# Performance work log

Hardware: AMD Instinct MI355X
Metric: run time of the kernel (lower is better)

Reference implementation:

```python
import jax, jax.numpy as jnp
import numpy as np

B, N0, N1, FD, L, H = 4, 256, 256, 128, 3, 1
NG = N0 + N1            # nodes per graph
N = B * NG              # total nodes
EPS_BN = 1e-5
EPS_SM = 1e-16


def _build_edges():
    def perm_edges(n, off):
        idx = np.arange(n)
        a = np.repeat(idx, n); b = np.tile(idx, n)
        m = a != b
        return np.stack([a[m], b[m]]) + off
    e_intra = np.concatenate([perm_edges(N0, 0), perm_edges(N1, N0)], axis=1)
    a = np.arange(N0); b = np.arange(N0, N0 + N1)
    cross1 = np.stack([np.repeat(a, N1), np.tile(b, N0)])
    cross2 = np.stack([np.repeat(b, N0), np.tile(a, N1)])
    eg = np.concatenate([e_intra, cross1, cross2], axis=1)
    tg = np.concatenate([np.zeros(e_intra.shape[1], np.int32),
                         np.ones(cross1.shape[1] + cross2.shape[1], np.int32)])
    ei = np.concatenate([eg + g * NG for g in range(B)], axis=1).astype(np.int32)
    et = np.tile(tg, B).astype(np.int32)
    return jnp.asarray(ei), jnp.asarray(et)


def setup_inputs() -> dict:
    key = jax.random.key(0)
    ks = jax.random.split(key, 8)
    edge_index, edge_type = _build_edges()
    return {
        'desc0': jax.random.normal(ks[0], (B, FD, N0), jnp.float32),
        'desc1': jax.random.normal(ks[1], (B, FD, N1), jnp.float32),
        'W': jax.random.normal(ks[2], (L, 2, FD, H * FD), jnp.float32) * (1.0 / np.sqrt(FD)),
        'q': jax.random.normal(ks[3], (L, H * FD, H), jnp.float32) * 0.1,
        'k': jax.random.normal(ks[4], (L, H * FD, H), jnp.float32) * 0.1,
        'conv_b': jnp.zeros((L, FD), jnp.float32),
        'lin_W': jax.random.normal(ks[5], (L, FD, 2 * FD), jnp.float32) * (1.0 / np.sqrt(2 * FD)),
        'lin_b': jnp.zeros((L, FD), jnp.float32),
        'gamma': jnp.ones((L, FD), jnp.float32),
        'beta': jnp.zeros((L, FD), jnp.float32),
        'edge_index': edge_index,
        'edge_type': edge_type,
    }


def _forward(desc0, desc1, W, q, k, conv_b, lin_W, lin_b, gamma, beta, edge_index, edge_type):
    # x: [B, NG, FD] -> flattened batch graph [N, FD]
    x = jnp.concatenate([desc0, desc1], axis=2)        # [B, FD, NG]
    x = jnp.transpose(x, (0, 2, 1)).reshape(N, FD)
    src, dst = edge_index[0], edge_index[1]
    nlayers = W.shape[0]
    heads = q.shape[2]
    for l in range(nlayers):
        # relation-specific node projections (equiv to per-edge bmm with weight[edge_type])
        proj = jnp.einsum('nf,rfo->nro', x, W[l])       # [N, 2, H*FD]
        out_i = proj[dst, edge_type]                    # [E, H*FD]
        out_j = proj[src, edge_type]                    # [E, H*FD]
        alpha = jax.nn.leaky_relu(out_i @ q[l] + out_j @ k[l], 0.2)  # [E, H]
        # softmax over incoming edges of each destination node (across-relation)
        amax = jax.ops.segment_max(alpha, dst, num_segments=N)
        ex = jnp.exp(alpha - amax[dst])
        denom = jax.ops.segment_sum(ex, dst, num_segments=N)
        att = ex / (denom[dst] + EPS_SM)                # [E, H]
        msg = (att[:, :, None] * out_j.reshape(-1, heads, FD)).reshape(-1, heads * FD)
        agg = jax.ops.segment_sum(msg, dst, num_segments=N).reshape(N, heads, FD)
        m1 = jax.nn.relu(agg.mean(axis=1) + conv_b[l])  # concat=False -> mean over heads
        m2 = jnp.concatenate([x, m1], axis=1) @ lin_W[l].T + lin_b[l]
        mu = m2.mean(axis=0)
        var = ((m2 - mu) ** 2).mean(axis=0)             # biased var (BatchNorm training)
        m3 = (m2 - mu) / jnp.sqrt(var + EPS_BN) * gamma[l] + beta[l]
        x = x + m3
    x = x.reshape(B, NG, FD).transpose(0, 2, 1)         # [B, FD, NG]
    return x


def reference(desc0, desc1, W, q, k, conv_b, lin_W, lin_b, gamma, beta, edge_index, edge_type):
    x = _forward(desc0, desc1, W, q, k, conv_b, lin_W, lin_b, gamma, beta, edge_index, edge_type)
    return x[:, :, :N0], x[:, :, N0:]
```

## Files before the change

kernel.cpp:

```cpp
#include <hip/hip_runtime.h>

#define FD  128
#define NN  2048

#define OFF_X     0
#define OFF_PROJ  262144
#define OFF_QS    786432
#define OFF_KS    790528
#define OFF_SUMS  794624
#define OFF_LWT   800768
#define OFF_M2    899072

__device__ __forceinline__ int swizzle_n0(int bid) {
    int g    = (bid & 7) >> 1;
    int slot = ((bid >> 3) << 1) | (bid & 1);
    return g*512 + slot*8;
}

__device__ __forceinline__ void proj_qsks8(
    const float* __restrict__ W, const float* __restrict__ qv,
    const float* __restrict__ kv, float* __restrict__ ws,
    int l, int n0, int t, const float (*xs)[FD],
    float (*redp)[256], float* red)
{
    int kh = t >> 8, tp = t & 255;
    int rsel = tp >> 7, o = tp & 127;
    const float* Wl = W + ((size_t)(l*2 + rsel)*FD)*FD + o;
    float acc[8];
#pragma unroll
    for (int r = 0; r < 8; r++) acc[r] = 0.f;
    int kbase = kh * 64;
#pragma unroll
    for (int kk = 0; kk < 64; kk += 4) {
        int k4 = kbase + kk;
        float w0 = Wl[(k4+0)*FD], w1 = Wl[(k4+1)*FD];
        float w2 = Wl[(k4+2)*FD], w3 = Wl[(k4+3)*FD];
#pragma unroll
        for (int r = 0; r < 8; r++) {
            float4 xq = *(const float4*)&xs[r][k4];
            acc[r] += xq.x*w0 + xq.y*w1 + xq.z*w2 + xq.w*w3;
        }
    }
    if (kh == 1) {
#pragma unroll
        for (int r = 0; r < 8; r++) redp[r][tp] = acc[r];
    }
    __syncthreads();
    if (t < 256) {
#pragma unroll
        for (int r = 0; r < 8; r++) acc[r] += redp[r][tp];
#pragma unroll
        for (int r = 0; r < 8; r++)
            ws[OFF_PROJ + (size_t)(n0 + r)*256 + tp] = acc[r];

        float qq = qv[l*FD + o], kq = kv[l*FD + o];
        int lane = t & 63, w = t >> 6;
#pragma unroll
        for (int r = 0; r < 8; r++) {
            float vq = acc[r]*qq, vk = acc[r]*kq;
            for (int off = 32; off; off >>= 1) {
                vq += __shfl_xor(vq, off, 64);
                vk += __shfl_xor(vk, off, 64);
            }
            if (lane == 0) { red[w*16 + r*2] = vq; red[w*16 + r*2 + 1] = vk; }
        }
    }
    __syncthreads();
    if (t < 32) {
        int r = t & 7, rs = (t >> 3) & 1, wh = t >> 4;
        float v = red[(rs*2)*16 + r*2 + wh] + red[(rs*2 + 1)*16 + r*2 + wh];
        if (wh == 0) ws[OFF_QS + rs*NN + n0 + r] = v;
        else         ws[OFF_KS + rs*NN + n0 + r] = v;
    }
}

__global__ __launch_bounds__(512, 2) void k_pre(
    const float* __restrict__ d0, const float* __restrict__ d1,
    const float* __restrict__ W,  const float* __restrict__ qv,
    const float* __restrict__ kv, const float* __restrict__ linW,
    float* __restrict__ ws)
{
    int bid = blockIdx.x, t = threadIdx.x;
    if (bid >= 256) {
        if (bid < 280) {
            int vb = bid - 256;
#pragma unroll
            for (int i = 0; i < 8; i++) {
                int e = vb*4096 + i*512 + t;
                int l = e >> 15, rem = e & 32767;
                int o = rem >> 8, c = rem & 255;
                ws[OFF_LWT + l*32768 + c*FD + o] = linW[e];
            }
        } else {
            for (int i = t; i < 6144; i += 512) ws[OFF_SUMS + i] = 0.f;
        }
        return;
    }
    __shared__ __attribute__((aligned(16))) float xs[8][FD];
    __shared__ float redp[8][256];
    __shared__ float red[64];
    int n0 = swizzle_n0(bid);
#pragma unroll
    for (int i = 0; i < 2; i++) {
        int idx = t + i*512;
        int row = idx >> 7, f = idx & 127;
        int n = n0 + row, gg = n >> 9, ii = n & 511;
        float v = (ii < 256) ? d0[gg*32768 + f*256 + ii]
                             : d1[gg*32768 + f*256 + (ii - 256)];
        xs[row][f] = v;
        ws[OFF_X + (size_t)n*FD + f] = v;
    }
    __syncthreads();
    proj_qsks8(W, qv, kv, ws, 0, n0, t, xs, redp, red);
}

__global__ __launch_bounds__(512, 2) void k_bp(
    const float* __restrict__ W,     const float* __restrict__ qv,
    const float* __restrict__ kv,    const float* __restrict__ gamma,
    const float* __restrict__ beta,  float* __restrict__ ws, int l)
{
    __shared__ float scale[FD], shift[FD];
    __shared__ __attribute__((aligned(16))) float xs[8][FD];
    __shared__ float redp[8][256];
    __shared__ float red[64];
    int bid = blockIdx.x, t = threadIdx.x;
    int lp = l - 1;
    if (t < 128) {
        float s0 = 0.f, s1 = 0.f;
#pragma unroll
        for (int sl = 0; sl < 8; sl++) {
            s0 += ws[OFF_SUMS + lp*2048 + sl*256 + t];
            s1 += ws[OFF_SUMS + lp*2048 + sl*256 + 128 + t];
        }
        float mu  = s0 * (1.f/2048.f);
        float var = s1 * (1.f/2048.f) - mu*mu;
        float rs  = rsqrtf(var + 1e-5f);
        float gm  = gamma[lp*FD + t], bt = beta[lp*FD + t];
        scale[t] = gm * rs;
        shift[t] = bt - mu * gm * rs;
    }
    __syncthreads();
    int n0 = swizzle_n0(bid);
#pragma unroll
    for (int i = 0; i < 2; i++) {
        int idx = t + i*512;
        int row = idx >> 7, f = idx & 127;
        size_t e = (size_t)(n0 + row)*FD + f;
        float xv = ws[OFF_X + e] + ws[OFF_M2 + e]*scale[f] + shift[f];
        xs[row][f] = xv;
        ws[OFF_X + e] = xv;
    }
    __syncthreads();
    proj_qsks8(W, qv, kv, ws, l, n0, t, xs, redp, red);
}

__global__ __launch_bounds__(512, 2) void k_attn(
    const float* __restrict__ convb, const float* __restrict__ linb,
    float* __restrict__ ws, int l)
{
    __shared__ __attribute__((aligned(16))) float att[8*512];
    __shared__ __attribute__((aligned(16))) float redB[8*8*128];
    __shared__ __attribute__((aligned(16))) float cat[8*256];
    __shared__ float r1[FD], r2[FD];

    int bid = blockIdx.x, t = threadIdx.x;
    int dstbase = swizzle_n0(bid);
    int g = dstbase >> 9, dloc0 = dstbase & 511;
    int Gd = (dloc0 >= 256) ? 1 : 0;

    {
        int d = t >> 6, p = t & 63;
        int dloc = dloc0 + d;
        float q0 = ws[OFF_QS + dstbase + d];
        float q1 = ws[OFF_QS + NN + dstbase + d];
        float sc[8];
#pragma unroll
        for (int j = 0; j < 8; j++) {
            int s = p + j*64;
            int ts = (s < 256) ? Gd : 1 - Gd;
            float a = (ts ? q1 : q0) + ws[OFF_KS + ts*NN + g*512 + s];
            a = a > 0.f ? a : 0.2f*a;
            sc[j] = (s == dloc) ? -1e30f : a;
        }
        float lm = sc[0];
#pragma unroll
        for (int j = 1; j < 8; j++) lm = fmaxf(lm, sc[j]);
        for (int off = 32; off; off >>= 1) lm = fmaxf(lm, __shfl_xor(lm, off, 64));
        float ex[8], lsum = 0.f;
#pragma unroll
        for (int j = 0; j < 8; j++) { ex[j] = __expf(sc[j] - lm); lsum += ex[j]; }
        for (int off = 32; off; off >>= 1) lsum += __shfl_xor(lsum, off, 64);
        float inv = 1.f / (lsum + 1e-16f);
#pragma unroll
        for (int j = 0; j < 8; j++) att[d*512 + p + j*64] = ex[j]*inv;
        if (t < 128) r1[t] = 0.f;
        else if (t < 256) r2[t - 128] = 0.f;
    }
    __syncthreads();

    int f4 = t & 31, sq = t >> 5;
    float acc[8][4];
#pragma unroll
    for (int d2 = 0; d2 < 8; d2++)
#pragma unroll
        for (int j = 0; j < 4; j++) acc[d2][j] = 0.f;
    {
        int ts = (sq < 8) ? Gd : 1 - Gd;
        const float* P = ws + OFF_PROJ + (size_t)(g*512)*256 + ts*128 + f4*4;
        int s0 = sq * 32;
        float4 bufA[4], bufB[4];
#pragma unroll
        for (int u = 0; u < 4; u++) bufA[u] = *(const float4*)&P[(size_t)(s0+u)*256];
#pragma unroll
        for (int ii = 0; ii < 8; ii++) {
            const float4* cur = (ii & 1) ? bufB : bufA;
            float4*       nxt = (ii & 1) ? bufA : bufB;
            if (ii < 7) {
#pragma unroll
                for (int u = 0; u < 4; u++)
                    nxt[u] = *(const float4*)&P[(size_t)(s0 + (ii+1)*4 + u)*256];
            }
#pragma unroll
            for (int u = 0; u < 4; u++) {
                int s = s0 + ii*4 + u;
                float4 p4 = cur[u];
#pragma unroll
                for (int d2 = 0; d2 < 8; d2++) {
                    float b = att[d2*512 + s];
                    acc[d2][0] += b*p4.x; acc[d2][1] += b*p4.y;
                    acc[d2][2] += b*p4.z; acc[d2][3] += b*p4.w;
                }
            }
        }
    }
    if (sq >= 8) {
#pragma unroll
        for (int d2 = 0; d2 < 8; d2++)
            *(float4*)&redB[((sq - 8)*8 + d2)*128 + f4*4] =
                make_float4(acc[d2][0], acc[d2][1], acc[d2][2], acc[d2][3]);
    }
    __syncthreads();
    if (sq < 8) {
#pragma unroll
        for (int d2 = 0; d2 < 8; d2++) {
            float4 p4 = *(const float4*)&redB[(sq*8 + d2)*128 + f4*4];
            *(float4*)&redB[(sq*8 + d2)*128 + f4*4] =
                make_float4(acc[d2][0]+p4.x, acc[d2][1]+p4.y, acc[d2][2]+p4.z, acc[d2][3]+p4.w);
        }
    }
    __syncthreads();

    {
        int dh = t >> 7, f = t & 127;
#pragma unroll
        for (int half = 0; half < 2; half++) {
            int d2 = dh + half*4;
            float agg = 0.f;
#pragma unroll
            for (int cc = 0; cc < 8; cc++) agg += redB[(cc*8 + d2)*128 + f];
            float m1v = fmaxf(agg + convb[l*FD + f], 0.f);
            cat[d2*256 + FD + f] = m1v;
            cat[d2*256 + f] = ws[OFF_X + (size_t)(dstbase + d2)*FD + f];
        }
    }
    __syncthreads();

#pragma unroll
    for (int d2 = 0; d2 < 8; d2++)
#pragma unroll
        for (int j = 0; j < 4; j++) acc[d2][j] = 0.f;
    {
        const float* lwt = ws + OFF_LWT + l*32768 + f4*4;
        int c0 = sq * 16;
        float4 bufA[4], bufB[4];
#pragma unroll
        for (int u = 0; u < 4; u++) bufA[u] = *(const float4*)&lwt[(c0+u)*128];
#pragma unroll
        for (int ii = 0; ii < 4; ii++) {
            const float4* cur = (ii & 1) ? bufB : bufA;
            float4*       nxt = (ii & 1) ? bufA : bufB;
            if (ii < 3) {
#pragma unroll
                for (int u = 0; u < 4; u++)
                    nxt[u] = *(const float4*)&lwt[(c0 + (ii+1)*4 + u)*128];
            }
#pragma unroll
            for (int u = 0; u < 4; u++) {
                int c = c0 + ii*4 + u;
                float4 w4 = cur[u];
#pragma unroll
                for (int d2 = 0; d2 < 8; d2++) {
                    float cv = cat[d2*256 + c];
                    acc[d2][0] += cv*w4.x; acc[d2][1] += cv*w4.y;
                    acc[d2][2] += cv*w4.z; acc[d2][3] += cv*w4.w;
                }
            }
        }
    }
    if (sq >= 8) {
#pragma unroll
        for (int d2 = 0; d2 < 8; d2++)
            *(float4*)&redB[((sq - 8)*8 + d2)*128 + f4*4] =
                make_float4(acc[d2][0], acc[d2][1], acc[d2][2], acc[d2][3]);
    }
    __syncthreads();
    if (sq < 8) {
#pragma unroll
        for (int d2 = 0; d2 < 8; d2++) {
            float4 p4 = *(const float4*)&redB[(sq*8 + d2)*128 + f4*4];
            *(float4*)&redB[(sq*8 + d2)*128 + f4*4] =
                make_float4(acc[d2][0]+p4.x, acc[d2][1]+p4.y, acc[d2][2]+p4.z, acc[d2][3]+p4.w);
        }
    }
    __syncthreads();

    {
        int dh = t >> 7, o = t & 127;
        float lb = linb[l*FD + o];
#pragma unroll
        for (int half = 0; half < 2; half++) {
            int d2 = dh + half*4;
            float m2v = lb;
#pragma unroll
            for (int cc = 0; cc < 8; cc++) m2v += redB[(cc*8 + d2)*128 + o];
            ws[OFF_M2 + (size_t)(dstbase + d2)*FD + o] = m2v;
            atomicAdd(&r1[o], m2v);
            atomicAdd(&r2[o], m2v*m2v);
        }
    }
    __syncthreads();
    if (t < 128) {
        int slot = bid & 7;
        atomicAdd(&ws[OFF_SUMS + l*2048 + slot*256 + t],       r1[t]);
        atomicAdd(&ws[OFF_SUMS + l*2048 + slot*256 + 128 + t], r2[t]);
    }
}

__global__ __launch_bounds__(256) void k_bnout(
    const float* __restrict__ gamma, const float* __restrict__ beta,
    float* __restrict__ ws, float* __restrict__ out)
{
    __shared__ float scale[FD], shift[FD];
    int bid = blockIdx.x, t = threadIdx.x;
    if (t < 128) {
        float s0 = 0.f, s1 = 0.f;
#pragma unroll
        for (int sl = 0; sl < 8; sl++) {
            s0 += ws[OFF_SUMS + 2*2048 + sl*256 + t];
            s1 += ws[OFF_SUMS + 2*2048 + sl*256 + 128 + t];
        }
        float mu  = s0 * (1.f/2048.f);
        float var = s1 * (1.f/2048.f) - mu*mu;
        float rs  = rsqrtf(var + 1e-5f);
        float gm  = gamma[2*FD + t], bt = beta[2*FD + t];
        scale[t] = gm * rs;
        shift[t] = bt - mu * gm * rs;
    }
    __syncthreads();
#pragma unroll
    for (int i = 0; i < 2; i++) {
        int idx = bid*512 + i*256 + t;
        int f = idx & 127, n = idx >> 7;
        float v = ws[OFF_X + idx] + ws[OFF_M2 + idx]*scale[f] + shift[f];
        int gg = n >> 9, ii = n & 511;
        int off = (ii < 256) ? (gg*32768 + f*256 + ii)
                             : (131072 + gg*32768 + f*256 + (ii - 256));
        out[off] = v;
    }
}

extern "C" void kernel_launch(void* const* d_in, const int* in_sizes, int n_in,
                              void* d_out, int out_size, void* d_ws, size_t ws_size,
                              hipStream_t stream) {
    (void)in_sizes; (void)n_in; (void)out_size; (void)ws_size;
    const float* desc0 = (const float*)d_in[0];
    const float* desc1 = (const float*)d_in[1];
    const float* W     = (const float*)d_in[2];
    const float* q     = (const float*)d_in[3];
    const float* kk    = (const float*)d_in[4];
    const float* convb = (const float*)d_in[5];
    const float* linW  = (const float*)d_in[6];
    const float* linb  = (const float*)d_in[7];
    const float* gamma = (const float*)d_in[8];
    const float* beta  = (const float*)d_in[9];
    float* ws  = (float*)d_ws;
    float* out = (float*)d_out;

    hipLaunchKernelGGL(k_pre,  dim3(281), dim3(512), 0, stream, desc0, desc1, W, q, kk, linW, ws);
    hipLaunchKernelGGL(k_attn, dim3(256), dim3(512), 0, stream, convb, linb, ws, 0);
    hipLaunchKernelGGL(k_bp,   dim3(256), dim3(512), 0, stream, W, q, kk, gamma, beta, ws, 1);
    hipLaunchKernelGGL(k_attn, dim3(256), dim3(512), 0, stream, convb, linb, ws, 1);
    hipLaunchKernelGGL(k_bp,   dim3(256), dim3(512), 0, stream, W, q, kk, gamma, beta, ws, 2);
    hipLaunchKernelGGL(k_attn, dim3(256), dim3(512), 0, stream, convb, linb, ws, 2);
    hipLaunchKernelGGL(k_bnout, dim3(512), dim3(256), 0, stream, gamma, beta, ws, out);
}
```

Baseline: 166.2 us.

## Fuse all layers into one cooperative persistent kernel with grid syncs

Replaces the seven separate launches with one cooperative kernel of 256 blocks that uses grid.sync between phases. Each block now keeps its node features and BatchNorm pre-activations in shared memory across layers instead of writing and re-reading them in global workspace. The goal is to remove per-launch overhead and global round trips for x and m2. The cost is grid-wide barriers, higher shared-memory use per block, and the requirement that all 256 blocks be co-resident.

Measured after the change: 370.5 us. 2.23x slower.

```diff
diff --git a/kernel.cpp b/kernel.cpp
--- a/kernel.cpp
+++ b/kernel.cpp
@@ -1,15 +1,16 @@
 #include <hip/hip_runtime.h>
+#include <hip/hip_cooperative_groups.h>
+
+namespace cg = cooperative_groups;
 
 #define FD  128
 #define NN  2048
 
-#define OFF_X     0
-#define OFF_PROJ  262144
-#define OFF_QS    786432
-#define OFF_KS    790528
-#define OFF_SUMS  794624
-#define OFF_LWT   800768
-#define OFF_M2    899072
+#define OFF_PROJ  0
+#define OFF_QS    524288
+#define OFF_KS    528384
+#define OFF_SUMS  532480
+#define OFF_LWT   538624
 
 __device__ __forceinline__ int swizzle_n0(int bid) {
     int g    = (bid & 7) >> 1;
@@ -74,274 +75,250 @@
     }
 }
 
-__global__ __launch_bounds__(512, 2) void k_pre(
-    const float* __restrict__ d0, const float* __restrict__ d1,
-    const float* __restrict__ W,  const float* __restrict__ qv,
-    const float* __restrict__ kv, const float* __restrict__ linW,
-    float* __restrict__ ws)
+__global__ __launch_bounds__(512, 2) void k_fused(
+    const float* __restrict__ d0,    const float* __restrict__ d1,
+    const float* __restrict__ W,     const float* __restrict__ qv,
+    const float* __restrict__ kv,    const float* __restrict__ convb,
+    const float* __restrict__ linW,  const float* __restrict__ linb,
+    const float* __restrict__ gamma, const float* __restrict__ beta,
+    float* __restrict__ ws,          float* __restrict__ out)
 {
-    int bid = blockIdx.x, t = threadIdx.x;
-    if (bid >= 256) {
-        if (bid < 280) {
-            int vb = bid - 256;
-#pragma unroll
-            for (int i = 0; i < 8; i++) {
-                int e = vb*4096 + i*512 + t;
-                int l = e >> 15, rem = e & 32767;
-                int o = rem >> 8, c = rem & 255;
-                ws[OFF_LWT + l*32768 + c*FD + o] = linW[e];
-            }
-        } else {
-            for (int i = t; i < 6144; i += 512) ws[OFF_SUMS + i] = 0.f;
-        }
-        return;
-    }
     __shared__ __attribute__((aligned(16))) float xs[8][FD];
+    __shared__ __attribute__((aligned(16))) float m2s[8][FD];
     __shared__ float redp[8][256];
     __shared__ float red[64];
-    int n0 = swizzle_n0(bid);
-#pragma unroll
-    for (int i = 0; i < 2; i++) {
-        int idx = t + i*512;
-        int row = idx >> 7, f = idx & 127;
-        int n = n0 + row, gg = n >> 9, ii = n & 511;
-        float v = (ii < 256) ? d0[gg*32768 + f*256 + ii]
-                             : d1[gg*32768 + f*256 + (ii - 256)];
-        xs[row][f] = v;
-        ws[OFF_X + (size_t)n*FD + f] = v;
-    }
-    __syncthreads();
-    proj_qsks8(W, qv, kv, ws, 0, n0, t, xs, redp, red);
-}
-
-__global__ __launch_bounds__(512, 2) void k_bp(
-    const float* __restrict__ W,     const float* __restrict__ qv,
-    const float* __restrict__ kv,    const float* __restrict__ gamma,
-    const float* __restrict__ beta,  float* __restrict__ ws, int l)
-{
     __shared__ float scale[FD], shift[FD];
-    __shared__ __attribute__((aligned(16))) float xs[8][FD];
-    __shared__ float redp[8][256];
-    __shared__ float red[64];
-    int bid = blockIdx.x, t = threadIdx.x;
-    int lp = l - 1;
-    if (t < 128) {
-        float s0 = 0.f, s1 = 0.f;
-#pragma unroll
-        for (int sl = 0; sl < 8; sl++) {
-            s0 += ws[OFF_SUMS + lp*2048 + sl*256 + t];
-            s1 += ws[OFF_SUMS + lp*2048 + sl*256 + 128 + t];
-        }
-        float mu  = s0 * (1.f/2048.f);
-        float var = s1 * (1.f/2048.f) - mu*mu;
-        float rs  = rsqrtf(var + 1e-5f);
-        float gm  = gamma[lp*FD + t], bt = beta[lp*FD + t];
-        scale[t] = gm * rs;
-        shift[t] = bt - mu * gm * rs;
-    }
-    __syncthreads();
-    int n0 = swizzle_n0(bid);
-#pragma unroll
-    for (int i = 0; i < 2; i++) {
-        int idx = t + i*512;
-        int row = idx >> 7, f = idx & 127;
-        size_t e = (size_t)(n0 + row)*FD + f;
-        float xv = ws[OFF_X + e] + ws[OFF_M2 + e]*scale[f] + shift[f];
-        xs[row][f] = xv;
-        ws[OFF_X + e] = xv;
-    }
-    __syncthreads();
-    proj_qsks8(W, qv, kv, ws, l, n0, t, xs, redp, red);
-}
-
-__global__ __launch_bounds__(512, 2) void k_attn(
-    const float* __restrict__ convb, const float* __restrict__ linb,
-    float* __restrict__ ws, int l)
-{
     __shared__ __attribute__((aligned(16))) float att[8*512];
     __shared__ __attribute__((aligned(16))) float redB[8*8*128];
-    __shared__ __attribute__((aligned(16))) float cat[8*256];
+    __shared__ __attribute__((aligned(16))) float m1s[8*FD];
     __shared__ float r1[FD], r2[FD];
 
+    cg::grid_group grid = cg::this_grid();
     int bid = blockIdx.x, t = threadIdx.x;
-    int dstbase = swizzle_n0(bid);
-    int g = dstbase >> 9, dloc0 = dstbase & 511;
+    int n0 = swizzle_n0(bid);
+    int g = n0 >> 9, dloc0 = n0 & 511;
     int Gd = (dloc0 >= 256) ? 1 : 0;
 
     {
-        int d = t >> 6, p = t & 63;
-        int dloc = dloc0 + d;
-        float q0 = ws[OFF_QS + dstbase + d];
-        float q1 = ws[OFF_QS + NN + dstbase + d];
-        float sc[8];
-#pragma unroll
-        for (int j = 0; j < 8; j++) {
-            int s = p + j*64;
-            int ts = (s < 256) ? Gd : 1 - Gd;
-            float a = (ts ? q1 : q0) + ws[OFF_KS + ts*NN + g*512 + s];
-            a = a > 0.f ? a : 0.2f*a;
-            sc[j] = (s == dloc) ? -1e30f : a;
-        }
-        float lm = sc[0];
-#pragma unroll
-        for (int j = 1; j < 8; j++) lm = fmaxf(lm, sc[j]);
-        for (int off = 32; off; off >>= 1) lm = fmaxf(lm, __shfl_xor(lm, off, 64));
-        float ex[8], lsum = 0.f;
-#pragma unroll
-        for (int j = 0; j < 8; j++) { ex[j] = __expf(sc[j] - lm); lsum += ex[j]; }
-        for (int off = 32; off; off >>= 1) lsum += __shfl_xor(lsum, off, 64);
-        float inv = 1.f / (lsum + 1e-16f);
-#pragma unroll
-        for (int j = 0; j < 8; j++) att[d*512 + p + j*64] = ex[j]*inv;
-        if (t < 128) r1[t] = 0.f;
-        else if (t < 256) r2[t - 128] = 0.f;
-    }
-    __syncthreads();
-
-    int f4 = t & 31, sq = t >> 5;
-    float acc[8][4];
-#pragma unroll
-    for (int d2 = 0; d2 < 8; d2++)
-#pragma unroll
-        for (int j = 0; j < 4; j++) acc[d2][j] = 0.f;
-    {
-        int ts = (sq < 8) ? Gd : 1 - Gd;
-        const float* P = ws + OFF_PROJ + (size_t)(g*512)*256 + ts*128 + f4*4;
-        int s0 = sq * 32;
-        float4 bufA[4], bufB[4];
-#pragma unroll
-        for (int u = 0; u < 4; u++) bufA[u] = *(const float4*)&P[(size_t)(s0+u)*256];
-#pragma unroll
-        for (int ii = 0; ii < 8; ii++) {
-            const float4* cur = (ii & 1) ? bufB : bufA;
-            float4*       nxt = (ii & 1) ? bufA : bufB;
-            if (ii < 7) {
-#pragma unroll
-                for (int u = 0; u < 4; u++)
-                    nxt[u] = *(const float4*)&P[(size_t)(s0 + (ii+1)*4 + u)*256];
-            }
-#pragma unroll
-            for (int u = 0; u < 4; u++) {
-                int s = s0 + ii*4 + u;
-                float4 p4 = cur[u];
+#pragma unroll
+        for (int i = 0; i < 2; i++) {
+            int idx = t + i*512;
+            int row = idx >> 7, f = idx & 127;
+            int n = n0 + row, gg = n >> 9, ii = n & 511;
+            xs[row][f] = (ii < 256) ? d0[gg*32768 + f*256 + ii]
+                                    : d1[gg*32768 + f*256 + (ii - 256)];
+        }
+        if (t < 384) {
+            int e = bid*384 + t;
+            int l = e >> 15, rem = e & 32767;
+            int o = rem >> 8, c = rem & 255;
+            ws[OFF_LWT + l*32768 + c*FD + o] = linW[e];
+        }
+        if (t < 24) ws[OFF_SUMS + bid*24 + t] = 0.f;
+        __syncthreads();
+        proj_qsks8(W, qv, kv, ws, 0, n0, t, xs, redp, red);
+    }
+    grid.sync();
+
+#pragma unroll 1
+    for (int l = 0; l < 3; l++) {
+        {
+            {
+                int d = t >> 6, p = t & 63;
+                int dloc = dloc0 + d;
+                float q0 = ws[OFF_QS + n0 + d];
+                float q1 = ws[OFF_QS + NN + n0 + d];
+                float sc[8];
+#pragma unroll
+                for (int j = 0; j < 8; j++) {
+                    int s = p + j*64;
+                    int ts = (s < 256) ? Gd : 1 - Gd;
+                    float a = (ts ? q1 : q0) + ws[OFF_KS + ts*NN + g*512 + s];
+                    a = a > 0.f ? a : 0.2f*a;
+                    sc[j] = (s == dloc) ? -1e30f : a;
+                }
+                float lm = sc[0];
+#pragma unroll
+                for (int j = 1; j < 8; j++) lm = fmaxf(lm, sc[j]);
+                for (int off = 32; off; off >>= 1) lm = fmaxf(lm, __shfl_xor(lm, off, 64));
+                float ex[8], lsum = 0.f;
+#pragma unroll
+                for (int j = 0; j < 8; j++) { ex[j] = __expf(sc[j] - lm); lsum += ex[j]; }
+                for (int off = 32; off; off >>= 1) lsum += __shfl_xor(lsum, off, 64);
+                float inv = 1.f / (lsum + 1e-16f);
+#pragma unroll
+                for (int j = 0; j < 8; j++) att[d*512 + p + j*64] = ex[j]*inv;
+                if (t < 128) r1[t] = 0.f;
+                else if (t < 256) r2[t - 128] = 0.f;
+            }
+            __syncthreads();
+
+            int f4 = t & 31, sq = t >> 5;
+            float acc[8][4];
+#pragma unroll
+            for (int d2 = 0; d2 < 8; d2++)
+#pragma unroll
+                for (int j = 0; j < 4; j++) acc[d2][j] = 0.f;
+            {
+                int ts = (sq < 8) ? Gd : 1 - Gd;
+                const float* P = ws + OFF_PROJ + (size_t)(g*512)*256 + ts*128 + f4*4;
+                int s0 = sq * 32;
+                float4 bufA[4], bufB[4];
+#pragma unroll
+                for (int u = 0; u < 4; u++) bufA[u] = *(const float4*)&P[(size_t)(s0+u)*256];
+#pragma unroll
+                for (int ii = 0; ii < 8; ii++) {
+                    const float4* cur = (ii & 1) ? bufB : bufA;
+                    float4*       nxt = (ii & 1) ? bufA : bufB;
+                    if (ii < 7) {
+#pragma unroll
+                        for (int u = 0; u < 4; u++)
+                            nxt[u] = *(const float4*)&P[(size_t)(s0 + (ii+1)*4 + u)*256];
+                    }
+#pragma unroll
+                    for (int u = 0; u < 4; u++) {
+                        int s = s0 + ii*4 + u;
+                        float4 p4 = cur[u];
+#pragma unroll
+                        for (int d2 = 0; d2 < 8; d2++) {
+                            float b = att[d2*512 + s];
+                            acc[d2][0] += b*p4.x; acc[d2][1] += b*p4.y;
+                            acc[d2][2] += b*p4.z; acc[d2][3] += b*p4.w;
+                        }
+                    }
+                }
+            }
+            if (sq >= 8) {
+#pragma unroll
+                for (int d2 = 0; d2 < 8; d2++)
+                    *(float4*)&redB[((sq - 8)*8 + d2)*128 + f4*4] =
+                        make_float4(acc[d2][0], acc[d2][1], acc[d2][2], acc[d2][3]);
+            }
+            __syncthreads();
+            if (sq < 8) {
 #pragma unroll
                 for (int d2 = 0; d2 < 8; d2++) {
-                    float b = att[d2*512 + s];
-                    acc[d2][0] += b*p4.x; acc[d2][1] += b*p4.y;
-                    acc[d2][2] += b*p4.z; acc[d2][3] += b*p4.w;
-                }
-            }
-        }
-    }
-    if (sq >= 8) {
-#pragma unroll
-        for (int d2 = 0; d2 < 8; d2++)
-            *(float4*)&redB[((sq - 8)*8 + d2)*128 + f4*4] =
-                make_float4(acc[d2][0], acc[d2][1], acc[d2][2], acc[d2][3]);
-    }
-    __syncthreads();
-    if (sq < 8) {
-#pragma unroll
-        for (int d2 = 0; d2 < 8; d2++) {
-            float4 p4 = *(const float4*)&redB[(sq*8 + d2)*128 + f4*4];
-            *(float4*)&redB[(sq*8 + d2)*128 + f4*4] =
-                make_float4(acc[d2][0]+p4.x, acc[d2][1]+p4.y, acc[d2][2]+p4.z, acc[d2][3]+p4.w);
-        }
-    }
-    __syncthreads();
-
-    {
-        int dh = t >> 7, f = t & 127;
-#pragma unroll
-        for (int half = 0; half < 2; half++) {
-            int d2 = dh + half*4;
-            float agg = 0.f;
-#pragma unroll
-            for (int cc = 0; cc < 8; cc++) agg += redB[(cc*8 + d2)*128 + f];
-            float m1v = fmaxf(agg + convb[l*FD + f], 0.f);
-            cat[d2*256 + FD + f] = m1v;
-            cat[d2*256 + f] = ws[OFF_X + (size_t)(dstbase + d2)*FD + f];
-        }
-    }
-    __syncthreads();
-
-#pragma unroll
-    for (int d2 = 0; d2 < 8; d2++)
-#pragma unroll
-        for (int j = 0; j < 4; j++) acc[d2][j] = 0.f;
-    {
-        const float* lwt = ws + OFF_LWT + l*32768 + f4*4;
-        int c0 = sq * 16;
-        float4 bufA[4], bufB[4];
-#pragma unroll
-        for (int u = 0; u < 4; u++) bufA[u] = *(const float4*)&lwt[(c0+u)*128];
-#pragma unroll
-        for (int ii = 0; ii < 4; ii++) {
-            const float4* cur = (ii & 1) ? bufB : bufA;
-            float4*       nxt = (ii & 1) ? bufA : bufB;
-            if (ii < 3) {
-#pragma unroll
-                for (int u = 0; u < 4; u++)
-                    nxt[u] = *(const float4*)&lwt[(c0 + (ii+1)*4 + u)*128];
-            }
-#pragma unroll
-            for (int u = 0; u < 4; u++) {
-                int c = c0 + ii*4 + u;
-                float4 w4 = cur[u];
+                    float4 p4 = *(const float4*)&redB[(sq*8 + d2)*128 + f4*4];
+                    *(float4*)&redB[(sq*8 + d2)*128 + f4*4] =
+                        make_float4(acc[d2][0]+p4.x, acc[d2][1]+p4.y, acc[d2][2]+p4.z, acc[d2][3]+p4.w);
+                }
+            }
+            __syncthreads();
+
+            {
+                int dh = t >> 7, f = t & 127;
+#pragma unroll
+                for (int half = 0; half < 2; half++) {
+                    int d2 = dh + half*4;
+                    float agg = 0.f;
+#pragma unroll
+                    for (int cc = 0; cc < 8; cc++) agg += redB[(cc*8 + d2)*128 + f];
+                    m1s[d2*FD + f] = fmaxf(agg + convb[l*FD + f], 0.f);
+                }
+            }
+            __syncthreads();
+
+#pragma unroll
+            for (int d2 = 0; d2 < 8; d2++)
+#pragma unroll
+                for (int j = 0; j < 4; j++) acc[d2][j] = 0.f;
+            {
+                const float* lwt = ws + OFF_LWT + l*32768 + f4*4;
+                const float* csrc = (sq < 8) ? &xs[0][0] : &m1s[0];
+                int c0 = sq * 16;
+                float4 bufA[4], bufB[4];
+#pragma unroll
+                for (int u = 0; u < 4; u++) bufA[u] = *(const float4*)&lwt[(c0+u)*128];
+#pragma unroll
+                for (int ii = 0; ii < 4; ii++) {
+                    const float4* cur = (ii & 1) ? bufB : bufA;
+                    float4*       nxt = (ii & 1) ? bufA : bufB;
+                    if (ii < 3) {
+#pragma unroll
+                        for (int u = 0; u < 4; u++)
+                            nxt[u] = *(const float4*)&lwt[(c0 + (ii+1)*4 + u)*128];
+                    }
+#pragma unroll
+                    for (int u = 0; u < 4; u++) {
+                        int c = c0 + ii*4 + u;
+                        float4 w4 = cur[u];
+#pragma unroll
+                        for (int d2 = 0; d2 < 8; d2++) {
+                            float cv = csrc[d2*FD + (c & 127)];
+                            acc[d2][0] += cv*w4.x; acc[d2][1] += cv*w4.y;
+                            acc[d2][2] += cv*w4.z; acc[d2][3] += cv*w4.w;
+                        }
+                    }
+                }
+            }
+            if (sq >= 8) {
+#pragma unroll
+                for (int d2 = 0; d2 < 8; d2++)
+                    *(float4*)&redB[((sq - 8)*8 + d2)*128 + f4*4] =
+                        make_float4(acc[d2][0], acc[d2][1], acc[d2][2], acc[d2][3]);
+            }
+            __syncthreads();
+            if (sq < 8) {
 #pragma unroll
                 for (int d2 = 0; d2 < 8; d2++) {
-                    float cv = cat[d2*256 + c];
-                    acc[d2][0] += cv*w4.x; acc[d2][1] += cv*w4.y;
-                    acc[d2][2] += cv*w4.z; acc[d2][3] += cv*w4.w;
-                }
-            }
-        }
-    }
-    if (sq >= 8) {
-#pragma unroll
-        for (int d2 = 0; d2 < 8; d2++)
-            *(float4*)&redB[((sq - 8)*8 + d2)*128 + f4*4] =
-                make_float4(acc[d2][0], acc[d2][1], acc[d2][2], acc[d2][3]);
-    }
-    __syncthreads();
-    if (sq < 8) {
-#pragma unroll
-        for (int d2 = 0; d2 < 8; d2++) {
-            float4 p4 = *(const float4*)&redB[(sq*8 + d2)*128 + f4*4];
-            *(float4*)&redB[(sq*8 + d2)*128 + f4*4] =
-                make_float4(acc[d2][0]+p4.x, acc[d2][1]+p4.y, acc[d2][2]+p4.z, acc[d2][3]+p4.w);
-        }
-    }
-    __syncthreads();
-
-    {
-        int dh = t >> 7, o = t & 127;
-        float lb = linb[l*FD + o];
-#pragma unroll
-        for (int half = 0; half < 2; half++) {
-            int d2 = dh + half*4;
-            float m2v = lb;
-#pragma unroll
-            for (int cc = 0; cc < 8; cc++) m2v += redB[(cc*8 + d2)*128 + o];
-            ws[OFF_M2 + (size_t)(dstbase + d2)*FD + o] = m2v;
-            atomicAdd(&r1[o], m2v);
-            atomicAdd(&r2[o], m2v*m2v);
-        }
-    }
-    __syncthreads();
-    if (t < 128) {
-        int slot = bid & 7;
-        atomicAdd(&ws[OFF_SUMS + l*2048 + slot*256 + t],       r1[t]);
-        atomicAdd(&ws[OFF_SUMS + l*2048 + slot*256 + 128 + t], r2[t]);
-    }
-}
-
-__global__ __launch_bounds__(256) void k_bnout(
-    const float* __restrict__ gamma, const float* __restrict__ beta,
-    float* __restrict__ ws, float* __restrict__ out)
-{
-    __shared__ float scale[FD], shift[FD];
-    int bid = blockIdx.x, t = threadIdx.x;
+                    float4 p4 = *(const float4*)&redB[(sq*8 + d2)*128 + f4*4];
+                    *(float4*)&redB[(sq*8 + d2)*128 + f4*4] =
+                        make_float4(acc[d2][0]+p4.x, acc[d2][1]+p4.y, acc[d2][2]+p4.z, acc[d2][3]+p4.w);
+                }
+            }
+            __syncthreads();
+
+            {
+                int dh = t >> 7, o = t & 127;
+                float lb = linb[l*FD + o];
+#pragma unroll
+                for (int half = 0; half < 2; half++) {
+                    int d2 = dh + half*4;
+                    float m2v = lb;
+#pragma unroll
+                    for (int cc = 0; cc < 8; cc++) m2v += redB[(cc*8 + d2)*128 + o];
+                    m2s[d2][o] = m2v;
+                    atomicAdd(&r1[o], m2v);
+                    atomicAdd(&r2[o], m2v*m2v);
+                }
+            }
+            __syncthreads();
+            if (t < 128) {
+                int slot = bid & 7;
+                atomicAdd(&ws[OFF_SUMS + l*2048 + slot*256 + t],       r1[t]);
+                atomicAdd(&ws[OFF_SUMS + l*2048 + slot*256 + 128 + t], r2[t]);
+            }
+        }
+        grid.sync();
+
+        if (l < 2) {
+            if (t < 128) {
+                float s0 = 0.f, s1 = 0.f;
+#pragma unroll
+                for (int sl = 0; sl < 8; sl++) {
+                    s0 += ws[OFF_SUMS + l*2048 + sl*256 + t];
+                    s1 += ws[OFF_SUMS + l*2048 + sl*256 + 128 + t];
+                }
+                float mu  = s0 * (1.f/2048.f);
+                float var = s1 * (1.f/2048.f) - mu*mu;
+                float rs  = rsqrtf(var + 1e-5f);
+                float gm  = gamma[l*FD + t], bt = beta[l*FD + t];
+                scale[t] = gm * rs;
+                shift[t] = bt - mu * gm * rs;
+            }
+            __syncthreads();
+#pragma unroll
+            for (int i = 0; i < 2; i++) {
+                int idx = t + i*512;
+                int row = idx >> 7, f = idx & 127;
+                xs[row][f] += m2s[row][f]*scale[f] + shift[f];
+            }
+            __syncthreads();
+            proj_qsks8(W, qv, kv, ws, l+1, n0, t, xs, redp, red);
+            grid.sync();
+        }
+    }
+
     if (t < 128) {
         float s0 = 0.f, s1 = 0.f;
 #pragma unroll
@@ -359,9 +336,10 @@
     __syncthreads();
 #pragma unroll
     for (int i = 0; i < 2; i++) {
-        int idx = bid*512 + i*256 + t;
-        int f = idx & 127, n = idx >> 7;
-        float v = ws[OFF_X + idx] + ws[OFF_M2 + idx]*scale[f] + shift[f];
+        int idx = t + i*512;
+        int row = idx >> 7, f = idx & 127;
+        int n = n0 + row;
+        float v = xs[row][f] + m2s[row][f]*scale[f] + shift[f];
         int gg = n >> 9, ii = n & 511;
         int off = (ii < 256) ? (gg*32768 + f*256 + ii)
                              : (131072 + gg*32768 + f*256 + (ii - 256));
@@ -386,11 +364,11 @@
     float* ws  = (float*)d_ws;
     float* out = (float*)d_out;
 
-    hipLaunchKernelGGL(k_pre,  dim3(281), dim3(512), 0, stream, desc0, desc1, W, q, kk, linW, ws);
-    hipLaunchKernelGGL(k_attn, dim3(256), dim3(512), 0, stream, convb, linb, ws, 0);
-    hipLaunchKernelGGL(k_bp,   dim3(256), dim3(512), 0, stream, W, q, kk, gamma, beta, ws, 1);
-    hipLaunchKernelGGL(k_attn, dim3(256), dim3(512), 0, stream, convb, linb, ws, 1);
-    hipLaunchKernelGGL(k_bp,   dim3(256), dim3(512), 0, stream, W, q, kk, gamma, beta, ws, 2);
-    hipLaunchKernelGGL(k_attn, dim3(256), dim3(512), 0, stream, convb, linb, ws, 2);
-    hipLaunchKernelGGL(k_bnout, dim3(512), dim3(256), 0, stream, gamma, beta, ws, out);
+    void* args[] = {
+        (void*)&desc0, (void*)&desc1, (void*)&W, (void*)&q, (void*)&kk,
+        (void*)&convb, (void*)&linW, (void*)&linb, (void*)&gamma, (void*)&beta,
+        (void*)&ws, (void*)&out
+    };
+    hipLaunchCooperativeKernel((const void*)k_fused, dim3(256), dim3(512),
+                               args, 0, stream);
 }
```

## Fold projection into attention by aggregating raw features then applying W

Applied to the files above, without the earlier changes.

Removes the separate per-layer projection kernels. Each layer kernel now computes q/k scores as dot products of x with precomputed W·q and W·k vectors, aggregates the un-projected (BN-applied) x rows weighted by attention per relation, and then multiplies the aggregated result by W. BatchNorm from the previous layer is applied on the fly, and x/m2 are ping-ponged between buffers. This cuts kernel launches and the proj write/read traffic, but each block now recomputes scores for the whole graph and does an extra small GEMM.

New measurement: 198.9 us. +19.7%, slower.

```diff
diff --git a/kernel.cpp b/kernel.cpp
--- a/kernel.cpp
+++ b/kernel.cpp
@@ -3,75 +3,19 @@
 #define FD  128
 #define NN  2048
 
-#define OFF_X     0
-#define OFF_PROJ  262144
-#define OFF_QS    786432
-#define OFF_KS    790528
-#define OFF_SUMS  794624
-#define OFF_LWT   800768
-#define OFF_M2    899072
+#define OFF_XA    0
+#define OFF_XB    262144
+#define OFF_M2A   524288
+#define OFF_M2B   786432
+#define OFF_SUMS  1048576
+#define OFF_LWT   1054720
+#define OFF_QH    1153024
+#define OFF_KH    1153792
 
 __device__ __forceinline__ int swizzle_n0(int bid) {
     int g    = (bid & 7) >> 1;
     int slot = ((bid >> 3) << 1) | (bid & 1);
     return g*512 + slot*8;
-}
-
-__device__ __forceinline__ void proj_qsks8(
-    const float* __restrict__ W, const float* __restrict__ qv,
-    const float* __restrict__ kv, float* __restrict__ ws,
-    int l, int n0, int t, const float (*xs)[FD],
-    float (*redp)[256], float* red)
-{
-    int kh = t >> 8, tp = t & 255;
-    int rsel = tp >> 7, o = tp & 127;
-    const float* Wl = W + ((size_t)(l*2 + rsel)*FD)*FD + o;
-    float acc[8];
-#pragma unroll
-    for (int r = 0; r < 8; r++) acc[r] = 0.f;
-    int kbase = kh * 64;
-#pragma unroll
-    for (int kk = 0; kk < 64; kk += 4) {
-        int k4 = kbase + kk;
-        float w0 = Wl[(k4+0)*FD], w1 = Wl[(k4+1)*FD];
-        float w2 = Wl[(k4+2)*FD], w3 = Wl[(k4+3)*FD];
-#pragma unroll
-        for (int r = 0; r < 8; r++) {
-            float4 xq = *(const float4*)&xs[r][k4];
-            acc[r] += xq.x*w0 + xq.y*w1 + xq.z*w2 + xq.w*w3;
-        }
-    }
-    if (kh == 1) {
-#pragma unroll
-        for (int r = 0; r < 8; r++) redp[r][tp] = acc[r];
-    }
-    __syncthreads();
-    if (t < 256) {
-#pragma unroll
-        for (int r = 0; r < 8; r++) acc[r] += redp[r][tp];
-#pragma unroll
-        for (int r = 0; r < 8; r++)
-            ws[OFF_PROJ + (size_t)(n0 + r)*256 + tp] = acc[r];
-
-        float qq = qv[l*FD + o], kq = kv[l*FD + o];
-        int lane = t & 63, w = t >> 6;
-#pragma unroll
-        for (int r = 0; r < 8; r++) {
-            float vq = acc[r]*qq, vk = acc[r]*kq;
-            for (int off = 32; off; off >>= 1) {
-                vq += __shfl_xor(vq, off, 64);
-                vk += __shfl_xor(vk, off, 64);
-            }
-            if (lane == 0) { red[w*16 + r*2] = vq; red[w*16 + r*2 + 1] = vk; }
-        }
-    }
-    __syncthreads();
-    if (t < 32) {
-        int r = t & 7, rs = (t >> 3) & 1, wh = t >> 4;
-        float v = red[(rs*2)*16 + r*2 + wh] + red[(rs*2 + 1)*16 + r*2 + wh];
-        if (wh == 0) ws[OFF_QS + rs*NN + n0 + r] = v;
-        else         ws[OFF_KS + rs*NN + n0 + r] = v;
-    }
 }
 
 __global__ __launch_bounds__(512, 2) void k_pre(
@@ -93,12 +37,20 @@
             }
         } else {
             for (int i = t; i < 6144; i += 512) ws[OFF_SUMS + i] = 0.f;
+#pragma unroll
+            for (int ii = 0; ii < 3; ii++) {
+                int e = ii*512 + t;
+                int sel = e & 1, idx = e >> 1;
+                const float* wrow = W + (size_t)idx*FD;
+                int l = idx >> 8;
+                const float* vvec = sel ? (kv + l*FD) : (qv + l*FD);
+                float acc = 0.f;
+                for (int o = 0; o < FD; o++) acc += wrow[o]*vvec[o];
+                ws[(sel ? OFF_KH : OFF_QH) + idx] = acc;
+            }
         }
         return;
     }
-    __shared__ __attribute__((aligned(16))) float xs[8][FD];
-    __shared__ float redp[8][256];
-    __shared__ float red[64];
     int n0 = swizzle_n0(bid);
 #pragma unroll
     for (int i = 0; i < 2; i++) {
@@ -107,78 +59,125 @@
         int n = n0 + row, gg = n >> 9, ii = n & 511;
         float v = (ii < 256) ? d0[gg*32768 + f*256 + ii]
                              : d1[gg*32768 + f*256 + (ii - 256)];
-        xs[row][f] = v;
-        ws[OFF_X + (size_t)n*FD + f] = v;
-    }
-    __syncthreads();
-    proj_qsks8(W, qv, kv, ws, 0, n0, t, xs, redp, red);
+        ws[OFF_XA + (size_t)n*FD + f] = v;
+    }
 }
 
-__global__ __launch_bounds__(512, 2) void k_bp(
-    const float* __restrict__ W,     const float* __restrict__ qv,
-    const float* __restrict__ kv,    const float* __restrict__ gamma,
-    const float* __restrict__ beta,  float* __restrict__ ws, int l)
-{
-    __shared__ float scale[FD], shift[FD];
-    __shared__ __attribute__((aligned(16))) float xs[8][FD];
-    __shared__ float redp[8][256];
-    __shared__ float red[64];
-    int bid = blockIdx.x, t = threadIdx.x;
-    int lp = l - 1;
-    if (t < 128) {
-        float s0 = 0.f, s1 = 0.f;
-#pragma unroll
-        for (int sl = 0; sl < 8; sl++) {
-            s0 += ws[OFF_SUMS + lp*2048 + sl*256 + t];
-            s1 += ws[OFF_SUMS + lp*2048 + sl*256 + 128 + t];
-        }
-        float mu  = s0 * (1.f/2048.f);
-        float var = s1 * (1.f/2048.f) - mu*mu;
-        float rs  = rsqrtf(var + 1e-5f);
-        float gm  = gamma[lp*FD + t], bt = beta[lp*FD + t];
-        scale[t] = gm * rs;
-        shift[t] = bt - mu * gm * rs;
-    }
-    __syncthreads();
-    int n0 = swizzle_n0(bid);
-#pragma unroll
-    for (int i = 0; i < 2; i++) {
-        int idx = t + i*512;
-        int row = idx >> 7, f = idx & 127;
-        size_t e = (size_t)(n0 + row)*FD + f;
-        float xv = ws[OFF_X + e] + ws[OFF_M2 + e]*scale[f] + shift[f];
-        xs[row][f] = xv;
-        ws[OFF_X + e] = xv;
-    }
-    __syncthreads();
-    proj_qsks8(W, qv, kv, ws, l, n0, t, xs, redp, red);
-}
-
-__global__ __launch_bounds__(512, 2) void k_attn(
-    const float* __restrict__ convb, const float* __restrict__ linb,
+template<int HASBN>
+__global__ __launch_bounds__(512, 2) void k_layer(
+    const float* __restrict__ Wg,    const float* __restrict__ convb,
+    const float* __restrict__ linb,  const float* __restrict__ gamma,
+    const float* __restrict__ beta,
+    const float* __restrict__ xin,   float* __restrict__ xout,
+    const float* __restrict__ m2in,  float* __restrict__ m2out,
     float* __restrict__ ws, int l)
 {
+    __shared__ float qkl[4*512];
     __shared__ __attribute__((aligned(16))) float att[8*512];
     __shared__ __attribute__((aligned(16))) float redB[8*8*128];
-    __shared__ __attribute__((aligned(16))) float cat[8*256];
+    __shared__ __attribute__((aligned(16))) float hgc[8*256];
+    __shared__ __attribute__((aligned(16))) float xs[8][FD];
+    __shared__ float scale[FD], shift[FD];
     __shared__ float r1[FD], r2[FD];
 
     int bid = blockIdx.x, t = threadIdx.x;
-    int dstbase = swizzle_n0(bid);
-    int g = dstbase >> 9, dloc0 = dstbase & 511;
+    int n0 = swizzle_n0(bid);
+    int g = n0 >> 9, dloc0 = n0 & 511;
     int Gd = (dloc0 >= 256) ? 1 : 0;
+
+    if (t < 128) {
+        r1[t] = 0.f;
+        if (HASBN) {
+            float s0 = 0.f, s1 = 0.f;
+#pragma unroll
+            for (int sl = 0; sl < 8; sl++) {
+                s0 += ws[OFF_SUMS + (l-1)*2048 + sl*256 + t];
+                s1 += ws[OFF_SUMS + (l-1)*2048 + sl*256 + 128 + t];
+            }
+            float mu  = s0 * (1.f/2048.f);
+            float var = s1 * (1.f/2048.f) - mu*mu;
+            float rs  = rsqrtf(var + 1e-5f);
+            float gm  = gamma[(l-1)*FD + t], bt = beta[(l-1)*FD + t];
+            scale[t] = gm * rs;
+            shift[t] = bt - mu * gm * rs;
+        }
+    } else if (t < 256) r2[t - 128] = 0.f;
+    __syncthreads();
+
+    {
+        int lane = t & 63, w = t >> 6;
+        int r8 = lane >> 3, fi = lane & 7;
+        int fb = fi*16;
+        float4 qh0[4], qh1[4], kh0[4], kh1[4], sc[4], sh[4];
+#pragma unroll
+        for (int j = 0; j < 4; j++) {
+            qh0[j] = *(const float4*)&ws[OFF_QH + l*256 +       fb + j*4];
+            qh1[j] = *(const float4*)&ws[OFF_QH + l*256 + 128 + fb + j*4];
+            kh0[j] = *(const float4*)&ws[OFF_KH + l*256 +       fb + j*4];
+            kh1[j] = *(const float4*)&ws[OFF_KH + l*256 + 128 + fb + j*4];
+            if (HASBN) {
+                sc[j] = *(const float4*)&scale[fb + j*4];
+                sh[j] = *(const float4*)&shift[fb + j*4];
+            }
+        }
+        const float* xg = xin  + (size_t)(g*512)*FD;
+        const float* mg = m2in + (size_t)(g*512)*FD;
+#pragma unroll 2
+        for (int it = 0; it < 8; it++) {
+            int s = w*64 + it*8 + r8;
+            float4 v4[4];
+#pragma unroll
+            for (int j = 0; j < 4; j++) {
+                float4 xq = *(const float4*)&xg[(size_t)s*FD + fb + j*4];
+                if (HASBN) {
+                    float4 mq = *(const float4*)&mg[(size_t)s*FD + fb + j*4];
+                    xq.x += mq.x*sc[j].x + sh[j].x;
+                    xq.y += mq.y*sc[j].y + sh[j].y;
+                    xq.z += mq.z*sc[j].z + sh[j].z;
+                    xq.w += mq.w*sc[j].w + sh[j].w;
+                }
+                v4[j] = xq;
+            }
+            float a0=0.f, a1=0.f, b0=0.f, b1=0.f;
+#pragma unroll
+            for (int j = 0; j < 4; j++) {
+                a0 += v4[j].x*qh0[j].x + v4[j].y*qh0[j].y + v4[j].z*qh0[j].z + v4[j].w*qh0[j].w;
+                a1 += v4[j].x*qh1[j].x + v4[j].y*qh1[j].y + v4[j].z*qh1[j].z + v4[j].w*qh1[j].w;
+                b0 += v4[j].x*kh0[j].x + v4[j].y*kh0[j].y + v4[j].z*kh0[j].z + v4[j].w*kh0[j].w;
+                b1 += v4[j].x*kh1[j].x + v4[j].y*kh1[j].y + v4[j].z*kh1[j].z + v4[j].w*kh1[j].w;
+            }
+            for (int m = 1; m <= 4; m <<= 1) {
+                a0 += __shfl_xor(a0, m, 64); a1 += __shfl_xor(a1, m, 64);
+                b0 += __shfl_xor(b0, m, 64); b1 += __shfl_xor(b1, m, 64);
+            }
+            if (fi == 0) {
+                qkl[0*512 + s] = a0; qkl[1*512 + s] = a1;
+                qkl[2*512 + s] = b0; qkl[3*512 + s] = b1;
+            }
+        }
+#pragma unroll
+        for (int i = 0; i < 2; i++) {
+            int idx = t + i*512;
+            int row = idx >> 7, f = idx & 127;
+            size_t e = (size_t)(n0 + row)*FD + f;
+            float v = xin[e];
+            if (HASBN) v += m2in[e]*scale[f] + shift[f];
+            xs[row][f] = v;
+        }
+    }
+    __syncthreads();
 
     {
         int d = t >> 6, p = t & 63;
         int dloc = dloc0 + d;
-        float q0 = ws[OFF_QS + dstbase + d];
-        float q1 = ws[OFF_QS + NN + dstbase + d];
+        float q0 = qkl[0*512 + dloc];
+        float q1 = qkl[1*512 + dloc];
         float sc[8];
 #pragma unroll
         for (int j = 0; j < 8; j++) {
             int s = p + j*64;
             int ts = (s < 256) ? Gd : 1 - Gd;
-            float a = (ts ? q1 : q0) + ws[OFF_KS + ts*NN + g*512 + s];
+            float a = (ts ? q1 : q0) + qkl[(2 + ts)*512 + s];
             a = a > 0.f ? a : 0.2f*a;
             sc[j] = (s == dloc) ? -1e30f : a;
         }
@@ -193,8 +192,6 @@
         float inv = 1.f / (lsum + 1e-16f);
 #pragma unroll
         for (int j = 0; j < 8; j++) att[d*512 + p + j*64] = ex[j]*inv;
-        if (t < 128) r1[t] = 0.f;
-        else if (t < 256) r2[t - 128] = 0.f;
     }
     __syncthreads();
 
@@ -205,30 +202,117 @@
 #pragma unroll
         for (int j = 0; j < 4; j++) acc[d2][j] = 0.f;
     {
-        int ts = (sq < 8) ? Gd : 1 - Gd;
-        const float* P = ws + OFF_PROJ + (size_t)(g*512)*256 + ts*128 + f4*4;
+        const float* xp = xin  + (size_t)(g*512)*FD + f4*4;
+        const float* mp = m2in + (size_t)(g*512)*FD + f4*4;
+        float4 sc4, sh4;
+        if (HASBN) {
+            sc4 = *(const float4*)&scale[f4*4];
+            sh4 = *(const float4*)&shift[f4*4];
+        }
         int s0 = sq * 32;
-        float4 bufA[4], bufB[4];
-#pragma unroll
-        for (int u = 0; u < 4; u++) bufA[u] = *(const float4*)&P[(size_t)(s0+u)*256];
+        float4 xA[4], xB[4], mA[4], mB[4];
+#pragma unroll
+        for (int u = 0; u < 4; u++) {
+            xA[u] = *(const float4*)&xp[(size_t)(s0+u)*FD];
+            if (HASBN) mA[u] = *(const float4*)&mp[(size_t)(s0+u)*FD];
+        }
 #pragma unroll
         for (int ii = 0; ii < 8; ii++) {
-            const float4* cur = (ii & 1) ? bufB : bufA;
-            float4*       nxt = (ii & 1) ? bufA : bufB;
+            const float4* curx = (ii & 1) ? xB : xA;
+            const float4* curm = (ii & 1) ? mB : mA;
+            float4* nxtx = (ii & 1) ? xA : xB;
+            float4* nxtm = (ii & 1) ? mA : mB;
             if (ii < 7) {
 #pragma unroll
-                for (int u = 0; u < 4; u++)
-                    nxt[u] = *(const float4*)&P[(size_t)(s0 + (ii+1)*4 + u)*256];
+                for (int u = 0; u < 4; u++) {
+                    nxtx[u] = *(const float4*)&xp[(size_t)(s0 + (ii+1)*4 + u)*FD];
+                    if (HASBN) nxtm[u] = *(const float4*)&mp[(size_t)(s0 + (ii+1)*4 + u)*FD];
+                }
             }
 #pragma unroll
             for (int u = 0; u < 4; u++) {
                 int s = s0 + ii*4 + u;
-                float4 p4 = cur[u];
+                float4 v = curx[u];
+                if (HASBN) {
+                    v.x += curm[u].x*sc4.x + sh4.x;
+                    v.y += curm[u].y*sc4.y + sh4.y;
+                    v.z += curm[u].z*sc4.z + sh4.z;
+                    v.w += curm[u].w*sc4.w + sh4.w;
+                }
 #pragma unroll
                 for (int d2 = 0; d2 < 8; d2++) {
                     float b = att[d2*512 + s];
-                    acc[d2][0] += b*p4.x; acc[d2][1] += b*p4.y;
-                    acc[d2][2] += b*p4.z; acc[d2][3] += b*p4.w;
+                    acc[d2][0] += b*v.x; acc[d2][1] += b*v.y;
+                    acc[d2][2] += b*v.z; acc[d2][3] += b*v.w;
+                }
+            }
+        }
+    }
+    {
+        int slot = (sq & 3) + ((sq >> 3) << 2);
+        if (sq & 4) {
+#pragma unroll
+            for (int d2 = 0; d2 < 8; d2++)
+                *(float4*)&redB[(slot*8 + d2)*128 + f4*4] =
+                    make_float4(acc[d2][0], acc[d2][1], acc[d2][2], acc[d2][3]);
+        }
+        __syncthreads();
+        if (!(sq & 4)) {
+#pragma unroll
+            for (int d2 = 0; d2 < 8; d2++) {
+                float4 p4 = *(const float4*)&redB[(slot*8 + d2)*128 + f4*4];
+                *(float4*)&redB[(slot*8 + d2)*128 + f4*4] =
+                    make_float4(acc[d2][0]+p4.x, acc[d2][1]+p4.y, acc[d2][2]+p4.z, acc[d2][3]+p4.w);
+            }
+        }
+        __syncthreads();
+    }
+
+    {
+        int dh = t >> 7, f = t & 127;
+#pragma unroll
+        for (int half = 0; half < 2; half++) {
+            int d2 = dh + half*4;
+            float hg0 = redB[(0*8+d2)*128+f] + redB[(1*8+d2)*128+f]
+                      + redB[(2*8+d2)*128+f] + redB[(3*8+d2)*128+f];
+            float hg1 = redB[(4*8+d2)*128+f] + redB[(5*8+d2)*128+f]
+                      + redB[(6*8+d2)*128+f] + redB[(7*8+d2)*128+f];
+            hgc[d2*256 + f]       = (Gd == 0) ? hg0 : hg1;
+            hgc[d2*256 + 128 + f] = (Gd == 0) ? hg1 : hg0;
+        }
+    }
+    __syncthreads();
+
+#pragma unroll
+    for (int d2 = 0; d2 < 8; d2++)
+#pragma unroll
+        for (int j = 0; j < 4; j++) acc[d2][j] = 0.f;
+    {
+        int rel = sq >> 3;
+        int c0m = (sq & 7) * 16;
+        const float* wp = Wg + ((size_t)(l*2 + rel)*FD + c0m)*FD + f4*4;
+        int c0 = sq * 16;
+        float4 wA[4], wB[4];
+#pragma unroll
+        for (int u = 0; u < 4; u++) wA[u] = *(const float4*)&wp[(size_t)u*FD];
+#pragma unroll
+        for (int ii = 0; ii < 4; ii++) {
+            const float4* cur = (ii & 1) ? wB : wA;
+            float4*       nxt = (ii & 1) ? wA : wB;
+            if (ii < 3) {
+#pragma unroll
+                for (int u = 0; u < 4; u++)
+                    nxt[u] = *(const float4*)&wp[(size_t)((ii+1)*4 + u)*FD];
+            }
+#pragma unroll
+            for (int u = 0; u < 4; u++) {
+                int c = c0 + ii*4 + u;
+                float4 w4 = cur[u];
+#pragma unroll
+                for (int d2 = 0; d2 < 8; d2++) {
+                    float cv = hgc[d2*256 + c];
+                    acc[d2][0] += cv*w4.x; acc[d2][1] += cv*w4.y;
+                    acc[d2][2] += cv*w4.z; acc[d2][3] += cv*w4.w;
                 }
             }
         }
@@ -258,9 +342,8 @@
             float agg = 0.f;
 #pragma unroll
             for (int cc = 0; cc < 8; cc++) agg += redB[(cc*8 + d2)*128 + f];
-            float m1v = fmaxf(agg + convb[l*FD + f], 0.f);
-            cat[d2*256 + FD + f] = m1v;
-            cat[d2*256 + f] = ws[OFF_X + (size_t)(dstbase + d2)*FD + f];
+            hgc[d2*256 + 128 + f] = fmaxf(agg + convb[l*FD + f], 0.f);
+            hgc[d2*256 + f] = xs[d2][f];
         }
     }
     __syncthreads();
@@ -272,13 +355,13 @@
     {
         const float* lwt = ws + OFF_LWT + l*32768 + f4*4;
         int c0 = sq * 16;
-        float4 bufA[4], bufB[4];
-#pragma unroll
-        for (int u = 0; u < 4; u++) bufA[u] = *(const float4*)&lwt[(c0+u)*128];
+        float4 wA[4], wB[4];
+#pragma unroll
+        for (int u = 0; u < 4; u++) wA[u] = *(const float4*)&lwt[(c0+u)*128];
 #pragma unroll
         for (int ii = 0; ii < 4; ii++) {
-            const float4* cur = (ii & 1) ? bufB : bufA;
-            float4*       nxt = (ii & 1) ? bufA : bufB;
+            const float4* cur = (ii & 1) ? wB : wA;
+            float4*       nxt = (ii & 1) ? wA : wB;
             if (ii < 3) {
 #pragma unroll
                 for (int u = 0; u < 4; u++)
@@ -290,7 +373,7 @@
                 float4 w4 = cur[u];
 #pragma unroll
                 for (int d2 = 0; d2 < 8; d2++) {
-                    float cv = cat[d2*256 + c];
+                    float cv = hgc[d2*256 + c];
                     acc[d2][0] += cv*w4.x; acc[d2][1] += cv*w4.y;
                     acc[d2][2] += cv*w4.z; acc[d2][3] += cv*w4.w;
                 }
@@ -323,7 +406,8 @@
             float m2v = lb;
 #pragma unroll
             for (int cc = 0; cc < 8; cc++) m2v += redB[(cc*8 + d2)*128 + o];
-            ws[OFF_M2 + (size_t)(dstbase + d2)*FD + o] = m2v;
+            m2out[(size_t)(n0 + d2)*FD + o] = m2v;
+            xout [(size_t)(n0 + d2)*FD + o] = xs[d2][o];
             atomicAdd(&r1[o], m2v);
             atomicAdd(&r2[o], m2v*m2v);
         }
@@ -361,7 +445,7 @@
     for (int i = 0; i < 2; i++) {
         int idx = bid*512 + i*256 + t;
         int f = idx & 127, n = idx >> 7;
-        float v = ws[OFF_X + idx] + ws[OFF_M2 + idx]*scale[f] + shift[f];
+        float v = ws[OFF_XB + idx] + ws[OFF_M2A + idx]*scale[f] + shift[f];
         int gg = n >> 9, ii = n & 511;
         int off = (ii < 256) ? (gg*32768 + f*256 + ii)
                              : (131072 + gg*32768 + f*256 + (ii - 256));
@@ -386,11 +470,19 @@
     float* ws  = (float*)d_ws;
     float* out = (float*)d_out;
 
-    hipLaunchKernelGGL(k_pre,  dim3(281), dim3(512), 0, stream, desc0, desc1, W, q, kk, linW, ws);
-    hipLaunchKernelGGL(k_attn, dim3(256), dim3(512), 0, stream, convb, linb, ws, 0);
-    hipLaunchKernelGGL(k_bp,   dim3(256), dim3(512), 0, stream, W, q, kk, gamma, beta, ws, 1);
-    hipLaunchKernelGGL(k_attn, dim3(256), dim3(512), 0, stream, convb, linb, ws, 1);
-    hipLaunchKernelGGL(k_bp,   dim3(256), dim3(512), 0, stream, W, q, kk, gamma, beta, ws, 2);
-    hipLaunchKernelGGL(k_attn, dim3(256), dim3(512), 0, stream, convb, linb, ws, 2);
-    hipLaunchKernelGGL(k_bnout, dim3(512), dim3(256), 0, stream, gamma, beta, ws, out);
+    float* xA  = ws + OFF_XA;
+    float* xB  = ws + OFF_XB;
+    float* m2A = ws + OFF_M2A;
+    float* m2B = ws + OFF_M2B;
+
+    hipLaunchKernelGGL(k_pre, dim3(281), dim3(512), 0, stream,
+                       desc0, desc1, W, q, kk, linW, ws);
+    hipLaunchKernelGGL((k_layer<0>), dim3(256), dim3(512), 0, stream,
+                       W, convb, linb, gamma, beta, xA, xB, m2B, m2A, ws, 0);
+    hipLaunchKernelGGL((k_layer<1>), dim3(256), dim3(512), 0, stream,
+                       W, convb, linb, gamma, beta, xB, xA, m2A, m2B, ws, 1);
+    hipLaunchKernelGGL((k_layer<1>), dim3(256), dim3(512), 0, stream,
+                       W, convb, linb, gamma, beta, xA, xB, m2B, m2A, ws, 2);
+    hipLaunchKernelGGL(k_bnout, dim3(512), dim3(256), 0, stream,
+                       gamma, beta, ws, out);
 }
```
